# Kernel optimization log

Hardware: AMD Instinct MI355X
Metric: run time of the kernel (lower is better)

The kernel has to match this reference:

```python
import jax, jax.numpy as jnp
import numpy as np

B, N, DPOS, F, P, K = 32, 1024, 3, 64, 128, 16


def setup_inputs() -> dict:
    key = jax.random.key(0)
    kp, kf, kw1, kw2 = jax.random.split(key, 4)
    points = jax.random.normal(kp, (B, N, DPOS), dtype=jnp.float32)
    features = jax.random.normal(kf, (B, N, F), dtype=jnp.float32)
    W1 = jax.random.normal(kw1, (2 * F, 2 * P), dtype=jnp.float32) * (1.0 / np.sqrt(2 * F))
    b1 = jnp.zeros((2 * P,), dtype=jnp.float32)
    W2 = jax.random.normal(kw2, (2 * P, P), dtype=jnp.float32) * (1.0 / np.sqrt(2 * P))
    b2 = jnp.zeros((P,), dtype=jnp.float32)
    return {"points": points, "features": features, "W1": W1, "b1": b1, "W2": W2, "b2": b2}


def reference(points, features, W1, b1, W2, b2):
    # pairwise squared distances: r_i - 2 p_i.p_j + r_j + 1e-5  -> [B, N, N]
    r = jnp.sum(points * points, axis=2, keepdims=True)
    m = jnp.einsum('bnd,bmd->bnm', points, points)
    D = r - 2.0 * m + jnp.swapaxes(r, 1, 2) + 1e-5
    # K+1 nearest (incl. self), drop self -> indices [B, N, K]
    _, idx = jax.lax.top_k(-D, K + 1)
    idx = idx[:, :, 1:]
    # gather neighbor features: [B, N, K, F]
    neighbors = features[jnp.arange(B)[:, None, None], idx]
    center = jnp.broadcast_to(features[:, :, None, :], neighbors.shape)
    local = jnp.concatenate([neighbors - center, center], axis=-1)  # [B,N,K,2F]
    # 2-layer MLP with exact GELU
    h = jax.nn.gelu(jnp.einsum('bnkf,fh->bnkh', local, W1) + b1, approximate=False)
    out = jax.nn.gelu(jnp.einsum('bnkh,hp->bnkp', h, W2) + b2, approximate=False)
    # mean over neighbors -> [B, N, P]
    return jnp.mean(out, axis=2)
```

## Files before the change

kernel.cpp:

```cpp
#include <hip/hip_runtime.h>
#include <math.h>

#define BB 32
#define NN 1024
#define FF 64
#define PP 128
#define KNN 16
#define H2 256
#define F2 128
#define KSEL 17
#define SVCAP 272

typedef float f32x4 __attribute__((ext_vector_type(4)));
typedef __bf16 bf16x8 __attribute__((ext_vector_type(8)));

__device__ __forceinline__ float gelu_fast(float x) {
    float s = x * x;
    float arg = x * fmaf(s, -0.1029438f, -2.3022115f);
    float e = __builtin_amdgcn_exp2f(arg);
    return x * __builtin_amdgcn_rcpf(1.0f + e);
}

__global__ __launch_bounds__(512, 8) void knn_prep(const float* __restrict__ points,
                                                   int* __restrict__ idx_out,
                                                   const float* __restrict__ W1,
                                                   const float* __restrict__ W2,
                                                   __bf16* __restrict__ Wcf,
                                                   __bf16* __restrict__ W2f) {
    if (blockIdx.x >= 4096) {
        int tid = (blockIdx.x - 4096) * 512 + threadIdx.x;
        if (tid < 4096) {
            const int lane = tid & 63, quad = lane >> 4, l16 = lane & 15;
            const int kk = (tid >> 6) & 1, n_tile = tid >> 7;
            const int n = n_tile * 16 + l16;
            const int kb = kk * 32 + quad * 8;
            bf16x8 v;
#pragma unroll
            for (int j = 0; j < 8; ++j) {
                const int k = kb + j;
                float x = (n < 256) ? W1[k * 256 + n]
                                    : (W1[(64 + k) * 256 + (n - 256)] - W1[k * 256 + (n - 256)]);
                v[j] = (__bf16)x;
            }
            *(bf16x8*)(Wcf + (size_t)tid * 8) = v;
        } else {
            const int t2 = tid - 4096;
            const int lane = t2 & 63, quad = lane >> 4, l16 = lane & 15;
            const int nt = (t2 >> 6) & 7, kk8 = t2 >> 9;
            const int p = nt * 16 + l16;
            const int hb = kk8 * 32 + quad * 8;
            bf16x8 v;
#pragma unroll
            for (int j = 0; j < 8; ++j) v[j] = (__bf16)W2[(size_t)(hb + j) * PP + p];
            *(bf16x8*)(W2f + (size_t)t2 * 8) = v;
        }
        return;
    }

    __shared__ float4 pts[NN];
    __shared__ unsigned sv_val[8][SVCAP];
    __shared__ unsigned sv_idx[8][SVCAP];
    __shared__ unsigned tie_idx[8][64];

    const int t = threadIdx.x;
    const int w = t >> 6, lane = t & 63;
    const int b = blockIdx.x >> 7;
    const int q0 = (blockIdx.x & 127) * 8;
    const float* pb = points + (size_t)b * NN * 3;
    const unsigned long long lt = (1ull << lane) - 1ull;

    for (int i = t; i < NN; i += 512) {
        float x = pb[3 * i], y = pb[3 * i + 1], z = pb[3 * i + 2];
        float r = __fadd_rn(__fadd_rn(__fmul_rn(x, x), __fmul_rn(y, y)), __fmul_rn(z, z));
        pts[i] = make_float4(x, y, z, r);
    }
    __syncthreads();

    const int qn = q0 + w;
    const int gq = b * NN + qn;
    const float4 qp = pts[qn];

    float D[16];
#pragma unroll
    for (int j = 0; j < 16; ++j) {
        float4 c = pts[j * 64 + lane];
        float dot = __fadd_rn(__fadd_rn(__fmul_rn(qp.x, c.x), __fmul_rn(qp.y, c.y)),
                              __fmul_rn(qp.z, c.z));
        D[j] = __fadd_rn(__fadd_rn(__fsub_rn(qp.w, __fmul_rn(2.0f, dot)), c.w), 1e-5f);
    }

    float mnf = D[0];
#pragma unroll
    for (int j = 1; j < 16; ++j) mnf = fminf(mnf, D[j]);
    const unsigned mbits = __float_as_uint(mnf);

    unsigned T = 0;
#pragma unroll
    for (int bit = 31; bit >= 0; --bit) {
        unsigned cand = T | (1u << bit);
        int cnt = __popcll(__ballot(mbits < cand));
        if (cnt < KSEL) T = cand;
    }

    unsigned base = 0;
#pragma unroll
    for (int j = 0; j < 16; ++j) {
        unsigned vb = __float_as_uint(D[j]);
        bool keep = (vb <= T);
        unsigned long long m = __ballot(keep);
        if (keep) {
            unsigned pos = base + (unsigned)__popcll(m & lt);
            if (pos < SVCAP) { sv_val[w][pos] = vb; sv_idx[w][pos] = j * 64 + lane; }
        }
        base += (unsigned)__popcll(m);
    }
    unsigned C = base > SVCAP ? SVCAP : base;
    const int S = (int)((C + 63) >> 6);

    unsigned Ts = 0;
    if (S == 1) {
        unsigned xv0 = (lane < (int)C) ? sv_val[w][lane] : 0xFFFFFFFFu;
#pragma unroll
        for (int bit = 31; bit >= 0; --bit) {
            unsigned cand = Ts | (1u << bit);
            int cnt = __popcll(__ballot(xv0 < cand));
            if (cnt < KSEL) Ts = cand;
        }
    } else {
        for (int bit = 31; bit >= 0; --bit) {
            unsigned cand = Ts | (1u << bit);
            int cnt = 0;
            for (int s = 0; s < S; ++s) {
                int i = s * 64 + lane;
                unsigned vb = (i < (int)C) ? sv_val[w][i] : 0xFFFFFFFFu;
                cnt += __popcll(__ballot(vb < cand));
            }
            if (cnt < KSEL) Ts = cand;
        }
    }

    int L = 0;
    for (int s = 0; s < S; ++s) {
        int i = s * 64 + lane;
        unsigned vb = (i < (int)C) ? sv_val[w][i] : 0xFFFFFFFFu;
        L += __popcll(__ballot(vb < Ts));
    }
    const int need = KSEL - L;

    unsigned vmin_l = 0xFFFFFFFFu;
    for (int s = 0; s < S; ++s) {
        int i = s * 64 + lane;
        unsigned vb = (i < (int)C) ? sv_val[w][i] : 0xFFFFFFFFu;
        vmin_l = vmin_l < vb ? vmin_l : vb;
    }
#pragma unroll
    for (int off = 32; off >= 1; off >>= 1) {
        unsigned o2 = __shfl_xor(vmin_l, off, 64);
        vmin_l = vmin_l < o2 ? vmin_l : o2;
    }
    const unsigned Vmin = vmin_l;
    unsigned imin_l = 0xFFFFFFFFu;
    for (int s = 0; s < S; ++s) {
        int i = s * 64 + lane;
        unsigned vb = (i < (int)C) ? sv_val[w][i] : 0xFFFFFFFFu;
        unsigned mi = (i < (int)C) ? sv_idx[w][i] : 0xFFFFFFFFu;
        if (vb == Vmin && mi < imin_l) imin_l = mi;
    }
#pragma unroll
    for (int off = 32; off >= 1; off >>= 1) {
        unsigned o2 = __shfl_xor(imin_l, off, 64);
        imin_l = imin_l < o2 ? imin_l : o2;
    }
    const unsigned dropIdx = imin_l;

    int* o = idx_out + (size_t)gq * KNN;
    unsigned wbase = 0, tbase = 0;
    for (int s = 0; s < S; ++s) {
        int i = s * 64 + lane;
        unsigned vb = (i < (int)C) ? sv_val[w][i] : 0xFFFFFFFFu;
        unsigned mi = (i < (int)C) ? sv_idx[w][i] : 0xFFFFFFFFu;
        bool wk = (vb < Ts) && (mi != dropIdx);
        unsigned long long wm = __ballot(wk);
        if (wk) o[wbase + (unsigned)__popcll(wm & lt)] = (int)mi;
        wbase += (unsigned)__popcll(wm);
        bool tk = (vb == Ts);
        unsigned long long tm2 = __ballot(tk);
        if (tk) {
            unsigned tp = tbase + (unsigned)__popcll(tm2 & lt);
            if (tp < 64) tie_idx[w][tp] = mi;
        }
        tbase += (unsigned)__popcll(tm2);
    }
    unsigned tc = tbase > 64 ? 64 : tbase;
    if ((int)tc == need) {
        bool tk = (lane < (int)tc);
        unsigned mi2 = tk ? tie_idx[w][lane] : 0xFFFFFFFFu;
        tk = tk && (mi2 != dropIdx);
        unsigned long long m3 = __ballot(tk);
        if (tk) o[wbase + (unsigned)__popcll(m3 & lt)] = (int)mi2;
    } else if (lane == 0) {
        unsigned pos = wbase;
        for (int r = 0; r < need; ++r) {
            unsigned best = 0xFFFFFFFFu; int bj = 0;
            for (int j2 = 0; j2 < (int)tc; ++j2) {
                unsigned mi = tie_idx[w][j2];
                if (mi < best) { best = mi; bj = j2; }
            }
            tie_idx[w][bj] = 0xFFFFFFFFu;
            if (best != dropIdx) o[pos++] = (int)best;
        }
    }
}

__global__ __launch_bounds__(256, 4) void gq_gemm(const float* __restrict__ feat,
                                                  const __bf16* __restrict__ Wcf,
                                                  const float* __restrict__ b1,
                                                  __bf16* __restrict__ Gall,
                                                  __bf16* __restrict__ Qall) {
    __shared__ __align__(16) __bf16 st[4][16][136];
    const int t = threadIdx.x, w = t >> 6, lane = t & 63;
    const int quad = lane >> 4, l16 = lane & 15;
    const int m0 = blockIdx.x * 16;

    bf16x8 a[2];
#pragma unroll
    for (int kk = 0; kk < 2; ++kk) {
        const float* ap = feat + (size_t)(m0 + l16) * 64 + kk * 32 + quad * 8;
        float4 a0 = *(const float4*)ap, a1 = *(const float4*)(ap + 4);
        bf16x8 v;
        v[0] = (__bf16)a0.x; v[1] = (__bf16)a0.y; v[2] = (__bf16)a0.z; v[3] = (__bf16)a0.w;
        v[4] = (__bf16)a1.x; v[5] = (__bf16)a1.y; v[6] = (__bf16)a1.z; v[7] = (__bf16)a1.w;
        a[kk] = v;
    }
    f32x4 acc[8];
#pragma unroll
    for (int nt = 0; nt < 8; ++nt) acc[nt] = (f32x4){0.f, 0.f, 0.f, 0.f};
#pragma unroll
    for (int kk = 0; kk < 2; ++kk)
#pragma unroll
        for (int nt = 0; nt < 8; ++nt) {
            bf16x8 bf = *(const bf16x8*)(Wcf + (size_t)(((w * 8 + nt) * 2 + kk) * 64 + lane) * 8);
            acc[nt] = __builtin_amdgcn_mfma_f32_16x16x32_bf16(a[kk], bf, acc[nt], 0, 0, 0);
        }

    const bool isQ = (w >= 2);
#pragma unroll
    for (int nt = 0; nt < 8; ++nt) {
        const int col = nt * 16 + l16;
        const float bias = isQ ? b1[(w - 2) * 128 + col] : 0.f;
#pragma unroll
        for (int r = 0; r < 4; ++r)
            st[w][quad * 4 + r][col] = (__bf16)(acc[nt][r] + bias);
    }
    __syncthreads();

    const int row = lane >> 2, c = lane & 3;
    const int m = m0 + row;
#pragma unroll
    for (int i = 0; i < 4; ++i) {
        const int col = c * 32 + i * 8;
        bf16x8 v = *(const bf16x8*)&st[w][row][col];
        if (!isQ) *(bf16x8*)(Gall + (size_t)m * H2 + w * 128 + col) = v;
        else      *(bf16x8*)(Qall + (size_t)m * H2 + (w - 2) * 128 + col) = v;
    }
}

__global__ __launch_bounds__(512, 6) void fused_mlp10(const __bf16* __restrict__ Gall,
                                                      const __bf16* __restrict__ Qall,
                                                      const int* __restrict__ knn_idx,
                                                      const __bf16* __restrict__ W2f,
                                                      const float* __restrict__ b2,
                                                      float* __restrict__ out) {
    __shared__ __align__(16) __bf16 w2s[8192];
    const int t = threadIdx.x, w = t >> 6, lane = t & 63;
    const int quad = lane >> 4, l16 = lane & 15;

    const int phys = blockIdx.x;
    const int blk = ((phys & 7) << 9) | (phys >> 3);

    const int q = blk * 8 + w;
    const int b = q >> 10;
    const int nb = knn_idx[q * KNN + l16];
    const __bf16* g0 = Gall + ((size_t)(b << 10) + nb) * H2;
    const __bf16* qq = Qall + (size_t)q * H2;

    f32x4 acc[8];
#pragma unroll
    for (int nt = 0; nt < 8; ++nt) acc[nt] = (f32x4){0.f, 0.f, 0.f, 0.f};

#pragma unroll
    for (int qtr = 0; qtr < 4; ++qtr) {
        if (qtr) __syncthreads();
#pragma unroll
        for (int i = 0; i < 2; ++i) {
            bf16x8 v = *(const bf16x8*)(W2f + (size_t)(qtr * 8192 + i * 4096 + t * 8));
            *(bf16x8*)&w2s[i * 4096 + t * 8] = v;
        }
        __syncthreads();

#pragma unroll
        for (int kl = 0; kl < 2; ++kl) {
            const int ho = (qtr * 2 + kl) * 32 + quad * 8;
            bf16x8 gA = *(const bf16x8*)(g0 + ho);
            bf16x8 qA = *(const bf16x8*)(qq + ho);
            bf16x8 a0;
#pragma unroll
            for (int j = 0; j < 8; ++j)
                a0[j] = (__bf16)gelu_fast((float)gA[j] + (float)qA[j]);
            const __bf16* bb = &w2s[kl * 4096 + lane * 8];
#pragma unroll
            for (int nt = 0; nt < 8; ++nt) {
                bf16x8 bf = *(const bf16x8*)(bb + nt * 512);
                acc[nt] = __builtin_amdgcn_mfma_f32_16x16x32_bf16(a0, bf, acc[nt], 0, 0, 0);
            }
        }
    }

#pragma unroll
    for (int nt = 0; nt < 8; ++nt) {
        const float bias = b2[nt * 16 + l16];
        float s = 0.f;
#pragma unroll
        for (int r = 0; r < 4; ++r) s += gelu_fast(acc[nt][r] + bias);
        s += __shfl_xor(s, 16, 64);
        s += __shfl_xor(s, 32, 64);
        if (quad == 0)
            out[(size_t)q * PP + nt * 16 + l16] = s * 0.0625f;
    }
}

extern "C" void kernel_launch(void* const* d_in, const int* in_sizes, int n_in,
                              void* d_out, int out_size, void* d_ws, size_t ws_size,
                              hipStream_t stream) {
    const float* points   = (const float*)d_in[0];
    const float* features = (const float*)d_in[1];
    const float* W1 = (const float*)d_in[2];
    const float* b1 = (const float*)d_in[3];
    const float* W2 = (const float*)d_in[4];
    const float* b2 = (const float*)d_in[5];
    float* out = (float*)d_out;

    const size_t IDX_B  = (size_t)BB * NN * KNN * 4;
    const size_t WCF_B  = 512 * 64 * 2;
    const size_t W2F_B  = 256 * 128 * 2;
    const size_t G_B    = (size_t)BB * NN * H2 * 2;

    int* knn_idx = (int*)d_ws;
    char* p = (char*)d_ws + IDX_B;
    __bf16* Wcf  = (__bf16*)p;  p += WCF_B;
    __bf16* W2f  = (__bf16*)p;  p += W2F_B;
    __bf16* Gall = (__bf16*)p;  p += G_B;
    __bf16* Qall = (__bf16*)p;

    knn_prep<<<4112, 512, 0, stream>>>(points, knn_idx, W1, W2, Wcf, W2f);
    gq_gemm<<<2048, 256, 0, stream>>>(features, Wcf, b1, Gall, Qall);
    fused_mlp10<<<4096, 512, 0, stream>>>(Gall, Qall, knn_idx, W2f, b2, out);
}
```

Before: 211.3 us.

## Fuse GQ GEMM blocks into KNN kernel and split weight prep into tiny kernel

```diff
diff --git a/kernel.cpp b/kernel.cpp
--- a/kernel.cpp
+++ b/kernel.cpp
@@ -21,46 +21,102 @@
     return x * __builtin_amdgcn_rcpf(1.0f + e);
 }
 
-__global__ __launch_bounds__(512, 8) void knn_prep(const float* __restrict__ points,
-                                                   int* __restrict__ idx_out,
-                                                   const float* __restrict__ W1,
-                                                   const float* __restrict__ W2,
-                                                   __bf16* __restrict__ Wcf,
-                                                   __bf16* __restrict__ W2f) {
+__global__ __launch_bounds__(512) void prep_frag(const float* __restrict__ W1,
+                                                 const float* __restrict__ W2,
+                                                 __bf16* __restrict__ Wcf,
+                                                 __bf16* __restrict__ W2f) {
+    int tid = blockIdx.x * 512 + threadIdx.x;
+    if (tid < 4096) {
+        const int lane = tid & 63, quad = lane >> 4, l16 = lane & 15;
+        const int kk = (tid >> 6) & 1, n_tile = tid >> 7;
+        const int n = n_tile * 16 + l16;
+        const int kb = kk * 32 + quad * 8;
+        bf16x8 v;
+#pragma unroll
+        for (int j = 0; j < 8; ++j) {
+            const int k = kb + j;
+            float x = (n < 256) ? W1[k * 256 + n]
+                                : (W1[(64 + k) * 256 + (n - 256)] - W1[k * 256 + (n - 256)]);
+            v[j] = (__bf16)x;
+        }
+        *(bf16x8*)(Wcf + (size_t)tid * 8) = v;
+    } else {
+        const int t2 = tid - 4096;
+        const int lane = t2 & 63, quad = lane >> 4, l16 = lane & 15;
+        const int nt = (t2 >> 6) & 7, kk8 = t2 >> 9;
+        const int p = nt * 16 + l16;
+        const int hb = kk8 * 32 + quad * 8;
+        bf16x8 v;
+#pragma unroll
+        for (int j = 0; j < 8; ++j) v[j] = (__bf16)W2[(size_t)(hb + j) * PP + p];
+        *(bf16x8*)(W2f + (size_t)t2 * 8) = v;
+    }
+}
+
+__global__ __launch_bounds__(512, 4) void knn_gq(const float* __restrict__ points,
+                                                 int* __restrict__ idx_out,
+                                                 const float* __restrict__ feat,
+                                                 const __bf16* __restrict__ Wcf,
+                                                 const float* __restrict__ b1,
+                                                 __bf16* __restrict__ Gall,
+                                                 __bf16* __restrict__ Qall) {
+    __shared__ __align__(16) unsigned char smem[35840];
+
     if (blockIdx.x >= 4096) {
-        int tid = (blockIdx.x - 4096) * 512 + threadIdx.x;
-        if (tid < 4096) {
-            const int lane = tid & 63, quad = lane >> 4, l16 = lane & 15;
-            const int kk = (tid >> 6) & 1, n_tile = tid >> 7;
-            const int n = n_tile * 16 + l16;
-            const int kb = kk * 32 + quad * 8;
+        __bf16* stb = (__bf16*)smem;
+        const int t = threadIdx.x, w8 = t >> 6, lane = t & 63;
+        const int quad = lane >> 4, l16 = lane & 15;
+        const int ws = w8 & 3;
+        const int m0 = (blockIdx.x - 4096) * 32 + (w8 >> 2) * 16;
+
+        bf16x8 a[2];
+#pragma unroll
+        for (int kk = 0; kk < 2; ++kk) {
+            const float* ap = feat + (size_t)(m0 + l16) * 64 + kk * 32 + quad * 8;
+            float4 a0 = *(const float4*)ap, a1 = *(const float4*)(ap + 4);
             bf16x8 v;
-#pragma unroll
-            for (int j = 0; j < 8; ++j) {
-                const int k = kb + j;
-                float x = (n < 256) ? W1[k * 256 + n]
-                                    : (W1[(64 + k) * 256 + (n - 256)] - W1[k * 256 + (n - 256)]);
-                v[j] = (__bf16)x;
+            v[0] = (__bf16)a0.x; v[1] = (__bf16)a0.y; v[2] = (__bf16)a0.z; v[3] = (__bf16)a0.w;
+            v[4] = (__bf16)a1.x; v[5] = (__bf16)a1.y; v[6] = (__bf16)a1.z; v[7] = (__bf16)a1.w;
+            a[kk] = v;
+        }
+        f32x4 acc[8];
+#pragma unroll
+        for (int nt = 0; nt < 8; ++nt) acc[nt] = (f32x4){0.f, 0.f, 0.f, 0.f};
+#pragma unroll
+        for (int kk = 0; kk < 2; ++kk)
+#pragma unroll
+            for (int nt = 0; nt < 8; ++nt) {
+                bf16x8 bf = *(const bf16x8*)(Wcf + (size_t)(((ws * 8 + nt) * 2 + kk) * 64 + lane) * 8);
+                acc[nt] = __builtin_amdgcn_mfma_f32_16x16x32_bf16(a[kk], bf, acc[nt], 0, 0, 0);
             }
-            *(bf16x8*)(Wcf + (size_t)tid * 8) = v;
-        } else {
-            const int t2 = tid - 4096;
-            const int lane = t2 & 63, quad = lane >> 4, l16 = lane & 15;
-            const int nt = (t2 >> 6) & 7, kk8 = t2 >> 9;
-            const int p = nt * 16 + l16;
-            const int hb = kk8 * 32 + quad * 8;
-            bf16x8 v;
-#pragma unroll
-            for (int j = 0; j < 8; ++j) v[j] = (__bf16)W2[(size_t)(hb + j) * PP + p];
-            *(bf16x8*)(W2f + (size_t)t2 * 8) = v;
+
+        const bool isQ = (ws >= 2);
+#pragma unroll
+        for (int nt = 0; nt < 8; ++nt) {
+            const int col = nt * 16 + l16;
+            const float bias = isQ ? b1[(ws - 2) * 128 + col] : 0.f;
+#pragma unroll
+            for (int r = 0; r < 4; ++r)
+                stb[(w8 * 16 + quad * 4 + r) * 136 + col] = (__bf16)(acc[nt][r] + bias);
+        }
+        __syncthreads();
+
+        const int row = lane >> 2, c = lane & 3;
+        const int m = m0 + row;
+#pragma unroll
+        for (int i = 0; i < 4; ++i) {
+            const int col = c * 32 + i * 8;
+            bf16x8 v = *(const bf16x8*)&stb[(w8 * 16 + row) * 136 + col];
+            if (!isQ) *(bf16x8*)(Gall + (size_t)m * H2 + ws * 128 + col) = v;
+            else      *(bf16x8*)(Qall + (size_t)m * H2 + (ws - 2) * 128 + col) = v;
         }
         return;
     }
 
-    __shared__ float4 pts[NN];
-    __shared__ unsigned sv_val[8][SVCAP];
-    __shared__ unsigned sv_idx[8][SVCAP];
-    __shared__ unsigned tie_idx[8][64];
+    float4*   pts     = (float4*)smem;
+    unsigned* sv_valb = (unsigned*)(smem + 16384);
+    unsigned* sv_idxb = (unsigned*)(smem + 25088);
+    unsigned* tie_b   = (unsigned*)(smem + 33792);
 
     const int t = threadIdx.x;
     const int w = t >> 6, lane = t & 63;
@@ -68,6 +124,9 @@
     const int q0 = (blockIdx.x & 127) * 8;
     const float* pb = points + (size_t)b * NN * 3;
     const unsigned long long lt = (1ull << lane) - 1ull;
+    unsigned* sv_val = sv_valb + w * SVCAP;
+    unsigned* sv_idx = sv_idxb + w * SVCAP;
+    unsigned* tie_idx = tie_b + w * 64;
 
     for (int i = t; i < NN; i += 512) {
         float x = pb[3 * i], y = pb[3 * i + 1], z = pb[3 * i + 2];
@@ -110,7 +169,7 @@
         unsigned long long m = __ballot(keep);
         if (keep) {
             unsigned pos = base + (unsigned)__popcll(m & lt);
-            if (pos < SVCAP) { sv_val[w][pos] = vb; sv_idx[w][pos] = j * 64 + lane; }
+            if (pos < SVCAP) { sv_val[pos] = vb; sv_idx[pos] = j * 64 + lane; }
         }
         base += (unsigned)__popcll(m);
     }
@@ -119,7 +178,7 @@
 
     unsigned Ts = 0;
     if (S == 1) {
-        unsigned xv0 = (lane < (int)C) ? sv_val[w][lane] : 0xFFFFFFFFu;
+        unsigned xv0 = (lane < (int)C) ? sv_val[lane] : 0xFFFFFFFFu;
 #pragma unroll
         for (int bit = 31; bit >= 0; --bit) {
             unsigned cand = Ts | (1u << bit);
@@ -132,7 +191,7 @@
             int cnt = 0;
             for (int s = 0; s < S; ++s) {
                 int i = s * 64 + lane;
-                unsigned vb = (i < (int)C) ? sv_val[w][i] : 0xFFFFFFFFu;
+                unsigned vb = (i < (int)C) ? sv_val[i] : 0xFFFFFFFFu;
                 cnt += __popcll(__ballot(vb < cand));
             }
             if (cnt < KSEL) Ts = cand;
@@ -142,7 +201,7 @@
     int L = 0;
     for (int s = 0; s < S; ++s) {
         int i = s * 64 + lane;
-        unsigned vb = (i < (int)C) ? sv_val[w][i] : 0xFFFFFFFFu;
+        unsigned vb = (i < (int)C) ? sv_val[i] : 0xFFFFFFFFu;
         L += __popcll(__ballot(vb < Ts));
     }
     const int need = KSEL - L;
@@ -150,7 +209,7 @@
     unsigned vmin_l = 0xFFFFFFFFu;
     for (int s = 0; s < S; ++s) {
         int i = s * 64 + lane;
-        unsigned vb = (i < (int)C) ? sv_val[w][i] : 0xFFFFFFFFu;
+        unsigned vb = (i < (int)C) ? sv_val[i] : 0xFFFFFFFFu;
         vmin_l = vmin_l < vb ? vmin_l : vb;
     }
 #pragma unroll
@@ -162,8 +221,8 @@
     unsigned imin_l = 0xFFFFFFFFu;
     for (int s = 0; s < S; ++s) {
         int i = s * 64 + lane;
-        unsigned vb = (i < (int)C) ? sv_val[w][i] : 0xFFFFFFFFu;
-        unsigned mi = (i < (int)C) ? sv_idx[w][i] : 0xFFFFFFFFu;
+        unsigned vb = (i < (int)C) ? sv_val[i] : 0xFFFFFFFFu;
+        unsigned mi = (i < (int)C) ? sv_idx[i] : 0xFFFFFFFFu;
         if (vb == Vmin && mi < imin_l) imin_l = mi;
     }
 #pragma unroll
@@ -177,8 +236,8 @@
     unsigned wbase = 0, tbase = 0;
     for (int s = 0; s < S; ++s) {
         int i = s * 64 + lane;
-        unsigned vb = (i < (int)C) ? sv_val[w][i] : 0xFFFFFFFFu;
-        unsigned mi = (i < (int)C) ? sv_idx[w][i] : 0xFFFFFFFFu;
+        unsigned vb = (i < (int)C) ? sv_val[i] : 0xFFFFFFFFu;
+        unsigned mi = (i < (int)C) ? sv_idx[i] : 0xFFFFFFFFu;
         bool wk = (vb < Ts) && (mi != dropIdx);
         unsigned long long wm = __ballot(wk);
         if (wk) o[wbase + (unsigned)__popcll(wm & lt)] = (int)mi;
@@ -187,14 +246,14 @@
         unsigned long long tm2 = __ballot(tk);
         if (tk) {
             unsigned tp = tbase + (unsigned)__popcll(tm2 & lt);
-            if (tp < 64) tie_idx[w][tp] = mi;
+            if (tp < 64) tie_idx[tp] = mi;
         }
         tbase += (unsigned)__popcll(tm2);
     }
     unsigned tc = tbase > 64 ? 64 : tbase;
     if ((int)tc == need) {
         bool tk = (lane < (int)tc);
-        unsigned mi2 = tk ? tie_idx[w][lane] : 0xFFFFFFFFu;
+        unsigned mi2 = tk ? tie_idx[lane] : 0xFFFFFFFFu;
         tk = tk && (mi2 != dropIdx);
         unsigned long long m3 = __ballot(tk);
         if (tk) o[wbase + (unsigned)__popcll(m3 & lt)] = (int)mi2;
@@ -203,65 +262,12 @@
         for (int r = 0; r < need; ++r) {
             unsigned best = 0xFFFFFFFFu; int bj = 0;
             for (int j2 = 0; j2 < (int)tc; ++j2) {
-                unsigned mi = tie_idx[w][j2];
+                unsigned mi = tie_idx[j2];
                 if (mi < best) { best = mi; bj = j2; }
             }
-            tie_idx[w][bj] = 0xFFFFFFFFu;
+            tie_idx[bj] = 0xFFFFFFFFu;
             if (best != dropIdx) o[pos++] = (int)best;
         }
-    }
-}
-
-__global__ __launch_bounds__(256, 4) void gq_gemm(const float* __restrict__ feat,
-                                                  const __bf16* __restrict__ Wcf,
-                                                  const float* __restrict__ b1,
-                                                  __bf16* __restrict__ Gall,
-                                                  __bf16* __restrict__ Qall) {
-    __shared__ __align__(16) __bf16 st[4][16][136];
-    const int t = threadIdx.x, w = t >> 6, lane = t & 63;
-    const int quad = lane >> 4, l16 = lane & 15;
-    const int m0 = blockIdx.x * 16;
-
-    bf16x8 a[2];
-#pragma unroll
-    for (int kk = 0; kk < 2; ++kk) {
-        const float* ap = feat + (size_t)(m0 + l16) * 64 + kk * 32 + quad * 8;
-        float4 a0 = *(const float4*)ap, a1 = *(const float4*)(ap + 4);
-        bf16x8 v;
-        v[0] = (__bf16)a0.x; v[1] = (__bf16)a0.y; v[2] = (__bf16)a0.z; v[3] = (__bf16)a0.w;
-        v[4] = (__bf16)a1.x; v[5] = (__bf16)a1.y; v[6] = (__bf16)a1.z; v[7] = (__bf16)a1.w;
-        a[kk] = v;
-    }
-    f32x4 acc[8];
-#pragma unroll
-    for (int nt = 0; nt < 8; ++nt) acc[nt] = (f32x4){0.f, 0.f, 0.f, 0.f};
-#pragma unroll
-    for (int kk = 0; kk < 2; ++kk)
-#pragma unroll
-        for (int nt = 0; nt < 8; ++nt) {
-            bf16x8 bf = *(const bf16x8*)(Wcf + (size_t)(((w * 8 + nt) * 2 + kk) * 64 + lane) * 8);
-            acc[nt] = __builtin_amdgcn_mfma_f32_16x16x32_bf16(a[kk], bf, acc[nt], 0, 0, 0);
-        }
-
-    const bool isQ = (w >= 2);
-#pragma unroll
-    for (int nt = 0; nt < 8; ++nt) {
-        const int col = nt * 16 + l16;
-        const float bias = isQ ? b1[(w - 2) * 128 + col] : 0.f;
-#pragma unroll
-        for (int r = 0; r < 4; ++r)
-            st[w][quad * 4 + r][col] = (__bf16)(acc[nt][r] + bias);
-    }
-    __syncthreads();
-
-    const int row = lane >> 2, c = lane & 3;
-    const int m = m0 + row;
-#pragma unroll
-    for (int i = 0; i < 4; ++i) {
-        const int col = c * 32 + i * 8;
-        bf16x8 v = *(const bf16x8*)&st[w][row][col];
-        if (!isQ) *(bf16x8*)(Gall + (size_t)m * H2 + w * 128 + col) = v;
-        else      *(bf16x8*)(Qall + (size_t)m * H2 + (w - 2) * 128 + col) = v;
     }
 }
 
@@ -352,7 +358,7 @@
     __bf16* Gall = (__bf16*)p;  p += G_B;
     __bf16* Qall = (__bf16*)p;
 
-    knn_prep<<<4112, 512, 0, stream>>>(points, knn_idx, W1, W2, Wcf, W2f);
-    gq_gemm<<<2048, 256, 0, stream>>>(features, Wcf, b1, Gall, Qall);
+    prep_frag<<<16, 512, 0, stream>>>(W1, W2, Wcf, W2f);
+    knn_gq<<<5120, 512, 0, stream>>>(points, knn_idx, features, Wcf, b1, Gall, Qall);
     fused_mlp10<<<4096, 512, 0, stream>>>(Gall, Qall, knn_idx, W2f, b2, out);
 }
```

After: 223.8 us. 1.06x slower.
